# Performance work log

Measured on AMD Instinct MI355X. Metric: run time of the kernel, lower is better.

Reference implementation:

```python
import jax, jax.numpy as jnp
import numpy as np

EPS = 1e-5  # torch LayerNorm default


def _layer_norm(x, w, b):
    # normalized_shape = [C, K, K] -> normalize over last 3 dims
    m = jnp.mean(x, axis=(-3, -2, -1), keepdims=True)
    v = jnp.var(x, axis=(-3, -2, -1), keepdims=True)
    return (x - m) * jax.lax.rsqrt(v + EPS) * w + b


def setup_inputs() -> dict:
    key = jax.random.key(0)
    k0, k1, k2, k3, k4, k5 = jax.random.split(key, 6)
    B, C, H, W, K = 32, 192, 56, 56, 7
    x = jax.random.normal(k0, (B, C, H, W), jnp.float32)
    ln0_w = jax.random.normal(k1, (C, K, K), jnp.float32)
    ln0_b = jax.random.normal(k2, (C, K, K), jnp.float32)
    conv0_w = jax.random.normal(k3, (C, 1, K, K), jnp.float32) * 0.1
    ln1_w = jax.random.normal(k4, (C, K, K), jnp.float32)
    ln1_b = jax.random.normal(k5, (C, K, K), jnp.float32)
    return {"x": x, "ln0_w": ln0_w, "ln0_b": ln0_b, "conv0_w": conv0_w,
            "ln1_w": ln1_w, "ln1_b": ln1_b}


def reference(x, ln0_w, ln0_b, conv0_w, ln1_w, ln1_b):
    B, C, H, W = x.shape
    K = conv0_w.shape[-1]
    # AdaptiveAvgPool2d((K,K)); H,W divisible by K -> uniform average pooling
    p = x.reshape(B, C, K, H // K, K, W // K).mean(axis=(3, 5))  # [B,C,K,K]
    p = _layer_norm(p, ln0_w, ln0_b)
    # depthwise KxK conv on KxK map, padding 'same'
    p = jax.lax.conv_general_dilated(
        p, conv0_w, window_strides=(1, 1), padding='SAME',
        dimension_numbers=('NCHW', 'OIHW', 'NCHW'), feature_group_count=C)
    p = jax.nn.relu(_layer_norm(p, ln1_w, ln1_b))  # [B,C,K,K] dynamic kernels
    # per-sample, per-channel depthwise conv: fold batch into channels
    ker = p.reshape(B * C, 1, K, K)
    out = jax.lax.conv_general_dilated(
        x.reshape(1, B * C, H, W), ker, window_strides=(1, 1), padding='SAME',
        dimension_numbers=('NCHW', 'OIHW', 'NCHW'), feature_group_count=B * C)
    return out.reshape(B, C, H, W)
```

## Files before the change

### kernel.cpp

```cpp
#include <hip/hip_runtime.h>

#define BB 32
#define CC 192
#define HH 56
#define WW 56
#define KS 7
#define HW 3136
#define KK 49
#define CKK 9408
#define PL 8
#define NCELL (BB * CC * KK)
#define NBC (BB * CC)
#define P0BLK 37
#define MIDBLK 24

typedef float f2 __attribute__((ext_vector_type(2)));

__global__ __launch_bounds__(256) void pool_kernel(const float* __restrict__ x,
                                                   float* __restrict__ p0,
                                                   float2* __restrict__ part0) {
    __shared__ float red[8];
    int b = blockIdx.x / P0BLK;
    int t = blockIdx.x - b * P0BLK;
    int cell = t * 256 + threadIdx.x;
    float v = 0.f;
    if (cell < CKK) {
        int c = cell / KK;
        int r = cell - c * KK;
        int i = r / KS;
        int j = r - i * KS;
        const float* src = x + ((size_t)(b * CC + c)) * HW + (i * PL) * WW + j * PL;
        float s = 0.f;
#pragma unroll
        for (int a = 0; a < PL; ++a) {
            float4 v0 = *(const float4*)(src + a * WW);
            float4 v1 = *(const float4*)(src + a * WW + 4);
            s += v0.x + v0.y + v0.z + v0.w + v1.x + v1.y + v1.z + v1.w;
        }
        v = s * (1.f / 64.f);
        p0[b * CKK + cell] = v;
    }
    float sv = v, sq = v * v;
#pragma unroll
    for (int o = 32; o > 0; o >>= 1) {
        sv += __shfl_down(sv, o, 64);
        sq += __shfl_down(sq, o, 64);
    }
    if ((threadIdx.x & 63) == 0) {
        red[(threadIdx.x >> 6) * 2 + 0] = sv;
        red[(threadIdx.x >> 6) * 2 + 1] = sq;
    }
    __syncthreads();
    if (threadIdx.x == 0)
        part0[blockIdx.x] = make_float2(red[0] + red[2] + red[4] + red[6],
                                        red[1] + red[3] + red[5] + red[7]);
}

__global__ __launch_bounds__(512) void mid_kernel(
    const float* __restrict__ p0,
    const float* __restrict__ ln0w, const float* __restrict__ ln0b,
    const float* __restrict__ w0,
    const float2* __restrict__ part0,
    float* __restrict__ q1,
    float2* __restrict__ part1)
{
    __shared__ float red[16];
    int tid  = threadIdx.x;
    int lane = tid & 63;
    int bc   = blockIdx.x * 8 + (tid >> 6);
    int b = bc / CC;
    int c = bc - b * CC;

    float s0 = 0.f, ss0 = 0.f;
    if (lane < P0BLK) {
        float2 p = part0[b * P0BLK + lane];
        s0 = p.x; ss0 = p.y;
    }
#pragma unroll
    for (int o = 32; o > 0; o >>= 1) {
        s0  += __shfl_down(s0, o, 64);
        ss0 += __shfl_down(ss0, o, 64);
    }
    s0  = __shfl(s0, 0, 64);
    ss0 = __shfl(ss0, 0, 64);
    float mean = s0 * (1.f / CKK);
    float rstd = rsqrtf(ss0 * (1.f / CKK) - mean * mean + 1e-5f);

    float val = 0.f;
    if (lane < KK)
        val = (p0[bc * KK + lane] - mean) * rstd * ln0w[c * KK + lane]
              + ln0b[c * KK + lane];

    int i0 = lane / KS;
    int j0 = lane - i0 * KS;
    const float* wc = w0 + c * KK;

    float acc = 0.f;
#pragma unroll
    for (int u = 0; u < KS; ++u) {
        int ii = i0 + u - 3;
#pragma unroll
        for (int v = 0; v < KS; ++v) {
            int jj = j0 + v - 3;
            bool ok = (ii >= 0) && (ii < KS) && (jj >= 0) && (jj < KS);
            int sl = ok ? (ii * KS + jj) : 0;
            float sv = __shfl(val, sl, 64);
            acc += ok ? sv * wc[u * KS + v] : 0.f;
        }
    }
    if (lane >= KK) acc = 0.f;
    if (lane < KK) q1[bc * KK + lane] = acc;

    float s2 = acc, ss2 = acc * acc;
#pragma unroll
    for (int o = 32; o > 0; o >>= 1) {
        s2  += __shfl_down(s2, o, 64);
        ss2 += __shfl_down(ss2, o, 64);
    }
    if (lane == 0) {
        red[(tid >> 6) * 2 + 0] = s2;
        red[(tid >> 6) * 2 + 1] = ss2;
    }
    __syncthreads();
    if (tid == 0) {
        float a = 0.f, q = 0.f;
#pragma unroll
        for (int w = 0; w < 8; ++w) { a += red[2 * w]; q += red[2 * w + 1]; }
        part1[blockIdx.x] = make_float2(a, q);
    }
}

__global__ __launch_bounds__(256) void tab_kernel(
    const float* __restrict__ q1, const float2* __restrict__ part1,
    const float* __restrict__ ln1w, const float* __restrict__ ln1b,
    f2* __restrict__ tab)
{
    int lane = threadIdx.x & 63;
    int bc   = blockIdx.x * 4 + (threadIdx.x >> 6);
    int b = bc / CC;
    int c = bc - b * CC;

    float s1 = 0.f, ss1 = 0.f;
    if (lane < MIDBLK) {
        float2 p = part1[b * MIDBLK + lane];
        s1 = p.x; ss1 = p.y;
    }
#pragma unroll
    for (int o = 32; o > 0; o >>= 1) {
        s1  += __shfl_down(s1, o, 64);
        ss1 += __shfl_down(ss1, o, 64);
    }
    s1  = __shfl(s1, 0, 64);
    ss1 = __shfl(ss1, 0, 64);
    float m = s1 * (1.f / CKK);
    float r = rsqrtf(ss1 * (1.f / CKK) - m * m + 1e-5f);

    float kt = 0.f;
    if (lane < KK) {
        float v = (q1[(size_t)bc * KK + lane] - m) * r * ln1w[c * KK + lane]
                  + ln1b[c * KK + lane];
        kt = v > 0.f ? v : 0.f;
    }

    int iA = 0, iB = 0;
    bool mA = false, mB = false;
    if (lane < 28) {
        int d = lane / KS, v = lane - KS * d;
        mA = (d < 3); iA = mA ? (2 * d + 1) * KS + v : 0;
        mB = (d > 0); iB = mB ? (2 * d - 1) * KS + v : 0;
    } else if (lane < 44) {
        int t = lane - 28;
        int d = t >> 2, j = t & 3;
        mA = true;     iA = 2 * d * KS + 2 * j;
        mB = (j < 3);  iB = mB ? 2 * d * KS + 2 * j + 1 : 0;
    }
    float va = __shfl(kt, iA, 64);
    float vb = __shfl(kt, iB, 64);
    f2 p;
    p.x = mA ? va : 0.f;
    p.y = mB ? vb : 0.f;

    f2* row = tab + (size_t)bc * 44;
    if (lane < 28)      row[16 + lane] = p;
    else if (lane < 44) row[lane - 28] = p;
}

#define TW2 64

__device__ __forceinline__ void pkfma_dl(f2& acc, f2 vp, f2 tp) {
    asm("v_pk_fma_f32 %0, %1, %2, %0 op_sel_hi:[1,0,1]"
        : "+v"(acc) : "v"(vp), "s"(tp));
}
__device__ __forceinline__ void pkfma_dh(f2& acc, f2 vp, f2 tp) {
    asm("v_pk_fma_f32 %0, %1, %2, %0 op_sel:[0,1,0] op_sel_hi:[1,1,1]"
        : "+v"(acc) : "v"(vp), "s"(tp));
}
__device__ __forceinline__ void pkfma_x(f2& acc, f2 vp, f2 tp) {
    asm("v_pk_fma_f32 %0, %1, %2, %0 op_sel:[1,0,0] op_sel_hi:[0,1,1]"
        : "+v"(acc) : "v"(vp), "s"(tp));
}

__global__ __launch_bounds__(256) void conv_kernel(
    const float* __restrict__ x,
    const f2* __restrict__ tab,
    float* __restrict__ out)
{
    __shared__ f2 tile2[32 * TW2];
    int bc   = blockIdx.x;
    int tid  = threadIdx.x;
    int lane = tid & 63;
    int wid  = tid >> 6;

    const float4* tb4 = (const float4*)(tab + (size_t)bc * 44);
    f2 dp[16], cpx[28];
#pragma unroll
    for (int i = 0; i < 8; ++i) {
        float4 t4 = tb4[i];
        dp[2 * i]     = (f2){t4.x, t4.y};
        dp[2 * i + 1] = (f2){t4.z, t4.w};
    }
#pragma unroll
    for (int i = 0; i < 14; ++i) {
        float4 t4 = tb4[8 + i];
        cpx[2 * i]     = (f2){t4.x, t4.y};
        cpx[2 * i + 1] = (f2){t4.z, t4.w};
    }

    const float* src = x + (size_t)bc * HW;
    int t0 = tid, t1 = tid + 256;
    int pr2a = 1 + t0 / 14, qa = t0 - (pr2a - 1) * 14;
    int pr2b = 1 + t1 / 14, qb = t1 - (pr2b - 1) * 14;
    int rAa = 2 * pr2a - 3, rBa = rAa + 1;
    int rAb = 2 * pr2b - 3, rBb = rAb + 1;
    float4 z4 = make_float4(0.f, 0.f, 0.f, 0.f);
    float4 a0 = (rAa >= 0) ? *(const float4*)(src + rAa * WW + 4 * qa) : z4;
    float4 b0 = (rBa < HH) ? *(const float4*)(src + rBa * WW + 4 * qa) : z4;
    float4 a1 = z4, b1 = z4;
    if (t1 < 29 * 14) {
        a1 = *(const float4*)(src + rAb * WW + 4 * qb);
        b1 = (rBb < HH) ? *(const float4*)(src + rBb * WW + 4 * qb) : z4;
    }

    if (tid < 128) {
        int pr2 = (tid < 64) ? 0 : 30;
        tile2[pr2 * TW2 + (tid & 63)] = (f2){0.f, 0.f};
    }
    if (tid < 232) {
        int pr2 = 1 + (tid >> 3);
        int c8  = tid & 7;
        int cell = (c8 < 3) ? c8 : 56 + c8;
        tile2[pr2 * TW2 + cell] = (f2){0.f, 0.f};
    }

    {
        f2* cell = tile2 + pr2a * TW2 + 3 + 4 * qa;
        cell[0] = (f2){a0.x, b0.x};
        cell[1] = (f2){a0.y, b0.y};
        cell[2] = (f2){a0.z, b0.z};
        cell[3] = (f2){a0.w, b0.w};
    }
    if (t1 < 29 * 14) {
        f2* cell = tile2 + pr2b * TW2 + 3 + 4 * qb;
        cell[0] = (f2){a1.x, b1.x};
        cell[1] = (f2){a1.y, b1.y};
        cell[2] = (f2){a1.z, b1.z};
        cell[3] = (f2){a1.w, b1.w};
    }
    __syncthreads();

    int r0 = wid * 14;
    const f2* base = tile2 + (wid * 7) * TW2 + lane;
    f2 acc2[7];
#pragma unroll
    for (int t = 0; t < 7; ++t) acc2[t] = (f2){0.f, 0.f};

    f2 va[KS], vb[KS];
#pragma unroll
    for (int j = 0; j < KS; ++j) va[j] = base[j];

#define CONV_STEP(S, CUR)                                              \
    {                                                                  \
        _Pragma("unroll")                                              \
        for (int d = 0; d < 4; ++d) {                                  \
            int t = (S) - d;                                           \
            if (t >= 0 && t <= 6) {                                    \
                _Pragma("unroll")                                      \
                for (int v = 0; v < KS; ++v) {                         \
                    if (v & 1) pkfma_dh(acc2[t], CUR[v], dp[d * 4 + (v >> 1)]); \
                    else       pkfma_dl(acc2[t], CUR[v], dp[d * 4 + (v >> 1)]); \
                    pkfma_x(acc2[t], CUR[v], cpx[d * KS + v]);         \
                }                                                      \
            }                                                          \
        }                                                              \
    }

#pragma unroll
    for (int ss = 0; ss < 5; ++ss) {
        int s0 = 2 * ss, s1 = 2 * ss + 1;
        {
            const f2* np = base + s1 * TW2;
#pragma unroll
            for (int j = 0; j < KS; ++j) vb[j] = np[j];
        }
        CONV_STEP(s0, va);
        if (ss < 4) {
            const f2* np = base + (s0 + 2) * TW2;
#pragma unroll
            for (int j = 0; j < KS; ++j) va[j] = np[j];
        }
        CONV_STEP(s1, vb);
    }
#undef CONV_STEP

    if (lane < WW) {
        float* ob = out + (size_t)bc * HW + r0 * WW + lane;
#pragma unroll
        for (int t = 0; t < 7; ++t) {
            ob[(2 * t) * WW]     = acc2[t].x;
            ob[(2 * t + 1) * WW] = acc2[t].y;
        }
    }
}

extern "C" void kernel_launch(void* const* d_in, const int* in_sizes, int n_in,
                              void* d_out, int out_size, void* d_ws, size_t ws_size,
                              hipStream_t stream) {
    const float* x    = (const float*)d_in[0];
    const float* ln0w = (const float*)d_in[1];
    const float* ln0b = (const float*)d_in[2];
    const float* w0   = (const float*)d_in[3];
    const float* ln1w = (const float*)d_in[4];
    const float* ln1b = (const float*)d_in[5];
    float* out = (float*)d_out;

    float*  p0    = (float*)d_ws;
    float*  q1    = p0 + NCELL;
    float2* part0 = (float2*)(q1 + NCELL);
    float2* part1 = part0 + BB * P0BLK;
    f2*     tab   = (f2*)(part1 + BB * MIDBLK);

    pool_kernel<<<BB * P0BLK, 256, 0, stream>>>(x, p0, part0);
    mid_kernel <<<BB * MIDBLK, 512, 0, stream>>>(p0, ln0w, ln0b, w0, part0, q1, part1);
    tab_kernel <<<NBC / 4, 256, 0, stream>>>(q1, part1, ln1w, ln1b, tab);
    conv_kernel<<<NBC, 256, 0, stream>>>(x, tab, out);
}
```

Before: 65.31 us.

## Process two channels per conv block, prefetching the second during first compute

Measured after the change: 64.93 us. About the same (-0.6%).

```diff
diff --git a/kernel.cpp b/kernel.cpp
--- a/kernel.cpp
+++ b/kernel.cpp
@@ -200,18 +200,68 @@
         : "+v"(acc) : "v"(vp), "s"(tp));
 }
 
-__global__ __launch_bounds__(256) void conv_kernel(
-    const float* __restrict__ x,
-    const f2* __restrict__ tab,
-    float* __restrict__ out)
-{
-    __shared__ f2 tile2[32 * TW2];
-    int bc   = blockIdx.x;
-    int tid  = threadIdx.x;
-    int lane = tid & 63;
-    int wid  = tid >> 6;
-
-    const float4* tb4 = (const float4*)(tab + (size_t)bc * 44);
+struct Task { int pr2a, qa, pr2b, qb; bool has1; };
+
+__device__ __forceinline__ Task task_decode(int tid) {
+    Task t;
+    int t0 = tid, t1 = tid + 256;
+    t.pr2a = 1 + t0 / 14; t.qa = t0 - (t.pr2a - 1) * 14;
+    t.pr2b = 1 + t1 / 14; t.qb = t1 - (t.pr2b - 1) * 14;
+    t.has1 = (t1 < 29 * 14);
+    return t;
+}
+
+__device__ __forceinline__ void stage_load(const float* __restrict__ src,
+                                           const Task& tk, float4& a0, float4& b0,
+                                           float4& a1, float4& b1) {
+    float4 z4 = make_float4(0.f, 0.f, 0.f, 0.f);
+    int rAa = 2 * tk.pr2a - 3, rBa = rAa + 1;
+    a0 = (rAa >= 0) ? *(const float4*)(src + rAa * WW + 4 * tk.qa) : z4;
+    b0 = (rBa < HH) ? *(const float4*)(src + rBa * WW + 4 * tk.qa) : z4;
+    a1 = z4; b1 = z4;
+    if (tk.has1) {
+        int rAb = 2 * tk.pr2b - 3, rBb = rAb + 1;
+        a1 = *(const float4*)(src + rAb * WW + 4 * tk.qb);
+        b1 = (rBb < HH) ? *(const float4*)(src + rBb * WW + 4 * tk.qb) : z4;
+    }
+}
+
+__device__ __forceinline__ void stage_write(f2* tile, const Task& tk,
+                                            const float4& a0, const float4& b0,
+                                            const float4& a1, const float4& b1) {
+    float4* c0 = (float4*)(tile + tk.pr2a * TW2 + 4 + 4 * tk.qa);
+    c0[0] = make_float4(a0.x, b0.x, a0.y, b0.y);
+    c0[1] = make_float4(a0.z, b0.z, a0.w, b0.w);
+    if (tk.has1) {
+        float4* c1 = (float4*)(tile + tk.pr2b * TW2 + 4 + 4 * tk.qb);
+        c1[0] = make_float4(a1.x, b1.x, a1.y, b1.y);
+        c1[1] = make_float4(a1.z, b1.z, a1.w, b1.w);
+    }
+}
+
+__device__ __forceinline__ void halo_zero(f2* t0, f2* t1, int tid) {
+    for (int i = tid; i < 360; i += 256) {
+        f2* tile = (i < 180) ? t0 : t1;
+        int r = (i < 180) ? i : i - 180;
+        int pr2, cell;
+        if (r < 116) {
+            pr2 = 1 + (r >> 2);
+            int p = r & 3;
+            cell = (p < 2) ? p * 2 : 60 + (p - 2) * 2;
+        } else {
+            int rr = r - 116;
+            pr2 = (rr < 32) ? 0 : 30;
+            cell = (rr & 31) * 2;
+        }
+        *(float4*)(tile + pr2 * TW2 + cell) = make_float4(0.f, 0.f, 0.f, 0.f);
+    }
+}
+
+__device__ __forceinline__ void compute_store(const f2* tile,
+                                              const f2* __restrict__ tabp,
+                                              float* __restrict__ ob,
+                                              int lane, int wid) {
+    const float4* tb4 = (const float4*)tabp;
     f2 dp[16], cpx[28];
 #pragma unroll
     for (int i = 0; i < 8; ++i) {
@@ -226,50 +276,8 @@
         cpx[2 * i + 1] = (f2){t4.z, t4.w};
     }
 
-    const float* src = x + (size_t)bc * HW;
-    int t0 = tid, t1 = tid + 256;
-    int pr2a = 1 + t0 / 14, qa = t0 - (pr2a - 1) * 14;
-    int pr2b = 1 + t1 / 14, qb = t1 - (pr2b - 1) * 14;
-    int rAa = 2 * pr2a - 3, rBa = rAa + 1;
-    int rAb = 2 * pr2b - 3, rBb = rAb + 1;
-    float4 z4 = make_float4(0.f, 0.f, 0.f, 0.f);
-    float4 a0 = (rAa >= 0) ? *(const float4*)(src + rAa * WW + 4 * qa) : z4;
-    float4 b0 = (rBa < HH) ? *(const float4*)(src + rBa * WW + 4 * qa) : z4;
-    float4 a1 = z4, b1 = z4;
-    if (t1 < 29 * 14) {
-        a1 = *(const float4*)(src + rAb * WW + 4 * qb);
-        b1 = (rBb < HH) ? *(const float4*)(src + rBb * WW + 4 * qb) : z4;
-    }
-
-    if (tid < 128) {
-        int pr2 = (tid < 64) ? 0 : 30;
-        tile2[pr2 * TW2 + (tid & 63)] = (f2){0.f, 0.f};
-    }
-    if (tid < 232) {
-        int pr2 = 1 + (tid >> 3);
-        int c8  = tid & 7;
-        int cell = (c8 < 3) ? c8 : 56 + c8;
-        tile2[pr2 * TW2 + cell] = (f2){0.f, 0.f};
-    }
-
-    {
-        f2* cell = tile2 + pr2a * TW2 + 3 + 4 * qa;
-        cell[0] = (f2){a0.x, b0.x};
-        cell[1] = (f2){a0.y, b0.y};
-        cell[2] = (f2){a0.z, b0.z};
-        cell[3] = (f2){a0.w, b0.w};
-    }
-    if (t1 < 29 * 14) {
-        f2* cell = tile2 + pr2b * TW2 + 3 + 4 * qb;
-        cell[0] = (f2){a1.x, b1.x};
-        cell[1] = (f2){a1.y, b1.y};
-        cell[2] = (f2){a1.z, b1.z};
-        cell[3] = (f2){a1.w, b1.w};
-    }
-    __syncthreads();
-
     int r0 = wid * 14;
-    const f2* base = tile2 + (wid * 7) * TW2 + lane;
+    const f2* base = tile + (wid * 7) * TW2 + lane + 1;
     f2 acc2[7];
 #pragma unroll
     for (int t = 0; t < 7; ++t) acc2[t] = (f2){0.f, 0.f};
@@ -313,13 +321,44 @@
 #undef CONV_STEP
 
     if (lane < WW) {
-        float* ob = out + (size_t)bc * HW + r0 * WW + lane;
 #pragma unroll
         for (int t = 0; t < 7; ++t) {
-            ob[(2 * t) * WW]     = acc2[t].x;
-            ob[(2 * t + 1) * WW] = acc2[t].y;
-        }
-    }
+            ob[(r0 + 2 * t) * WW + lane]     = acc2[t].x;
+            ob[(r0 + 2 * t + 1) * WW + lane] = acc2[t].y;
+        }
+    }
+}
+
+__global__ __launch_bounds__(256) void conv_kernel(
+    const float* __restrict__ x,
+    const f2* __restrict__ tab,
+    float* __restrict__ out)
+{
+    __shared__ f2 tiles[2][32 * TW2];
+    int tid  = threadIdx.x;
+    int lane = tid & 63;
+    int wid  = tid >> 6;
+    int chA  = blockIdx.x * 2;
+    int chB  = chA + 1;
+
+    Task tk = task_decode(tid);
+    float4 a0, b0, a1, b1;
+
+    stage_load(x + (size_t)chA * HW, tk, a0, b0, a1, b1);
+    halo_zero(tiles[0], tiles[1], tid);
+    stage_write(tiles[0], tk, a0, b0, a1, b1);
+    __syncthreads();
+
+    stage_load(x + (size_t)chB * HW, tk, a0, b0, a1, b1);
+    __builtin_amdgcn_sched_barrier(0);
+
+    compute_store(tiles[0], tab + (size_t)chA * 44, out + (size_t)chA * HW,
+                  lane, wid);
+
+    stage_write(tiles[1], tk, a0, b0, a1, b1);
+    __syncthreads();
+    compute_store(tiles[1], tab + (size_t)chB * 44, out + (size_t)chB * HW,
+                  lane, wid);
 }
 
 extern "C" void kernel_launch(void* const* d_in, const int* in_sizes, int n_in,
@@ -342,5 +381,5 @@
     pool_kernel<<<BB * P0BLK, 256, 0, stream>>>(x, p0, part0);
     mid_kernel <<<BB * MIDBLK, 512, 0, stream>>>(p0, ln0w, ln0b, w0, part0, q1, part1);
     tab_kernel <<<NBC / 4, 256, 0, stream>>>(q1, part1, ln1w, ln1b, tab);
-    conv_kernel<<<NBC, 256, 0, stream>>>(x, tab, out);
-}
+    conv_kernel<<<NBC / 2, 256, 0, stream>>>(x, tab, out);
+}
```
